# Kernel optimization log

Measured on AMD Instinct MI355X. Metric: run time of the kernel, lower is better.

The kernel has to match this reference:

```python
import jax, jax.numpy as jnp
import numpy as np

N = 1048576
C = 128

def setup_inputs() -> dict:
    key = jax.random.key(0)
    k1, k2 = jax.random.split(key)
    # probabilities must be positive for log; uniform in (1e-6, 1)
    predicts = jax.random.uniform(k1, (N, C), dtype=jnp.float32, minval=1e-6, maxval=1.0)
    labels = jax.random.randint(k2, (N,), 0, C, dtype=jnp.int64)
    return {"predicts": predicts, "labels": labels}

def reference(predicts, labels):
    # loss = -(1/N) * sum_i log(predicts[i, labels[i]])
    labels = labels.reshape(-1)
    picked = jnp.take_along_axis(predicts, labels[:, None], axis=1)[:, 0]  # [N]
    return -jnp.mean(jnp.log(picked))
```

## Files before the change

### kernel.cpp

```cpp
#include <hip/hip_runtime.h>

#define BLOCK 256
#define PER_THREAD 4
#define C 128

__global__ __launch_bounds__(BLOCK) void MultiCrossEntropyLoss_kernel(
    const float* __restrict__ predicts,
    const int* __restrict__ labels,
    float* __restrict__ out,
    int n, float inv_n)
{
    const int tid = blockIdx.x * BLOCK + threadIdx.x;
    const int i0 = tid * PER_THREAD;

    float s = 0.0f;
    if (i0 + PER_THREAD - 1 < n) {
        int4 lab = *reinterpret_cast<const int4*>(labels + i0);
        float p0 = predicts[(i0 + 0) * C + lab.x];
        float p1 = predicts[(i0 + 1) * C + lab.y];
        float p2 = predicts[(i0 + 2) * C + lab.z];
        float p3 = predicts[(i0 + 3) * C + lab.w];
        s = __logf(p0) + __logf(p1) + __logf(p2) + __logf(p3);
    } else {
        for (int i = i0; i < n; ++i) {
            s += __logf(predicts[i * C + labels[i]]);
        }
    }

    #pragma unroll
    for (int off = 32; off > 0; off >>= 1) {
        s += __shfl_down(s, off, 64);
    }

    __shared__ float wave_sums[BLOCK / 64];
    const int lane = threadIdx.x & 63;
    const int wv   = threadIdx.x >> 6;
    if (lane == 0) wave_sums[wv] = s;
    __syncthreads();

    if (threadIdx.x == 0) {
        float bs = wave_sums[0] + wave_sums[1] + wave_sums[2] + wave_sums[3];
        atomicAdd(out, -bs * inv_n);
    }
}

extern "C" void kernel_launch(void* const* d_in, const int* in_sizes, int n_in,
                              void* d_out, int out_size, void* d_ws, size_t ws_size,
                              hipStream_t stream) {
    const float* predicts = (const float*)d_in[0];
    const int*   labels   = (const int*)d_in[1];
    float*       out      = (float*)d_out;
    const int n = in_sizes[1];

    hipMemsetAsync(d_out, 0, sizeof(float), stream);

    const int per_block = BLOCK * PER_THREAD;
    const int grid = (n + per_block - 1) / per_block;
    MultiCrossEntropyLoss_kernel<<<grid, BLOCK, 0, stream>>>(
        predicts, labels, out, n, 1.0f / (float)n);
}
```

Before: 598.3 us.

## Stream full prediction matrix coalesced instead of gathering per-row label elements

Replaces the per-row scattered gather of one float per row with a grid-stride loop that reads the whole predictions matrix as coalesced float4 loads. Each thread keeps only the element whose float4 slot matches the row's label and accumulates its log. The grid is capped and made persistent. This trades many latency-bound scattered loads for reading every byte of the matrix at full bandwidth, so total traffic grows in exchange for fully coalesced access.

```diff
diff --git a/kernel.cpp b/kernel.cpp
--- a/kernel.cpp
+++ b/kernel.cpp
@@ -1,36 +1,36 @@
 #include <hip/hip_runtime.h>
 
 #define BLOCK 256
-#define PER_THREAD 4
 #define C 128
+#define F4_PER_ROW (C / 4)
+#define GRID_CAP 2048
 
 __global__ __launch_bounds__(BLOCK) void MultiCrossEntropyLoss_kernel(
-    const float* __restrict__ predicts,
-    const int* __restrict__ labels,
-    float* __restrict__ out,
-    int n, float inv_n)
+    const float4* __restrict__ predicts4,
+    const int*    __restrict__ labels,
+    float*        __restrict__ out,
+    int total4, float inv_n)
 {
-    const int tid = blockIdx.x * BLOCK + threadIdx.x;
-    const int i0 = tid * PER_THREAD;
+    const int tid    = blockIdx.x * BLOCK + threadIdx.x;
+    const int stride = gridDim.x * BLOCK;
+    const int slot   = tid & 31;
 
     float s = 0.0f;
-    if (i0 + PER_THREAD - 1 < n) {
-        int4 lab = *reinterpret_cast<const int4*>(labels + i0);
-        float p0 = predicts[(i0 + 0) * C + lab.x];
-        float p1 = predicts[(i0 + 1) * C + lab.y];
-        float p2 = predicts[(i0 + 2) * C + lab.z];
-        float p3 = predicts[(i0 + 3) * C + lab.w];
-        s = __logf(p0) + __logf(p1) + __logf(p2) + __logf(p3);
-    } else {
-        for (int i = i0; i < n; ++i) {
-            s += __logf(predicts[i * C + labels[i]]);
+    #pragma unroll 4
+    for (int idx = tid; idx < total4; idx += stride) {
+        const float4 v   = predicts4[idx];
+        const int    lab = labels[idx >> 5];
+        if ((lab >> 2) == slot) {
+            const float x01 = (lab & 1) ? v.y : v.x;
+            const float x23 = (lab & 1) ? v.w : v.z;
+            const float x   = (lab & 2) ? x23 : x01;
+            s += __logf(x);
         }
     }
 
     #pragma unroll
-    for (int off = 32; off > 0; off >>= 1) {
+    for (int off = 32; off > 0; off >>= 1)
         s += __shfl_down(s, off, 64);
-    }
 
     __shared__ float wave_sums[BLOCK / 64];
     const int lane = threadIdx.x & 63;
@@ -54,8 +54,9 @@
 
     hipMemsetAsync(d_out, 0, sizeof(float), stream);
 
-    const int per_block = BLOCK * PER_THREAD;
-    const int grid = (n + per_block - 1) / per_block;
+    const int total4 = n * F4_PER_ROW;
+    int grid = (total4 + BLOCK - 1) / BLOCK;
+    if (grid > GRID_CAP) grid = GRID_CAP;
     MultiCrossEntropyLoss_kernel<<<grid, BLOCK, 0, stream>>>(
-        predicts, labels, out, n, 1.0f / (float)n);
+        (const float4*)predicts, labels, out, total4, 1.0f / (float)n);
 }
```

New measurement: 653.7 us. 1.09x slower.
